# Performance work log

Measured on AMD Instinct MI355X. Metric: run time of the kernel, lower is better.

## Reference

```python
import jax, jax.numpy as jnp
import numpy as np

N_NODES = 714
LRELU = 0.01   # nn.LeakyReLU default
GAT_SLOPE = 0.2  # PyG GATConv internal leaky_relu slope


def _gcn_conv(x, row, col, W, b, n):
    # PyG GCNConv: h = x W; sym-normalized aggregation over edges (self loops already appended)
    h = x @ W
    ones = jnp.ones(row.shape[0], h.dtype)
    deg = jax.ops.segment_sum(ones, col, num_segments=n)
    dinv = jnp.where(deg > 0, jax.lax.rsqrt(deg), 0.0)
    norm = dinv[row] * dinv[col]
    out = jax.ops.segment_sum(h[row] * norm[:, None], col, num_segments=n)
    return out + b


def _gat_conv(x, row, col, W, a_src, a_dst, b, n):
    # PyG GATConv, heads=1: h = x W (no lin bias); edge score = leaky_relu(a_src.h_j + a_dst.h_i)
    h = x @ W
    asrc = h @ a_src
    adst = h @ a_dst
    e = jax.nn.leaky_relu(asrc[row] + adst[col], GAT_SLOPE)
    emax = jax.ops.segment_max(e, col, num_segments=n)
    ee = jnp.exp(e - emax[col])
    denom = jax.ops.segment_sum(ee, col, num_segments=n)
    alpha = ee / (denom[col] + 1e-16)
    out = jax.ops.segment_sum(h[row] * alpha[:, None], col, num_segments=n)
    return out + b


def _forward(feature, edges, poi_tab, cat_tab, lat_tab, long_tab,
             W_in, b_in, gat_W, gat_asrc, gat_adst, gat_b,
             W_out, b_out, W_fc1, b_fc1, W_fc2, b_fc2):
    B, n, _ = feature.shape
    # embedding lookups, concat -> [B, n, 800]
    x = jnp.concatenate([
        poi_tab[feature[..., 0]],
        cat_tab[feature[..., 1]],
        lat_tab[feature[..., 3]],
        long_tab[feature[..., 4]],
    ], axis=-1)
    # append self loops (both GCNConv and GATConv add them by default)
    sl = jnp.arange(n, dtype=edges.dtype)
    sl2 = jnp.broadcast_to(jnp.stack([sl, sl])[None], (B, 2, n))
    ei = jnp.concatenate([edges, sl2], axis=2)  # [B, 2, E+n]
    lrelu = lambda t: jax.nn.leaky_relu(t, LRELU)

    def per_graph(xg, eg):
        row, col = eg[0], eg[1]
        h = lrelu(_gcn_conv(xg, row, col, W_in, b_in, n))
        for i in range(gat_W.shape[0]):  # 3 AGCNUnits, each reuses ONE GATConv twice
            t = _gat_conv(h, row, col, gat_W[i], gat_asrc[i], gat_adst[i], gat_b[i], n)
            h = lrelu(t) + t
            h = lrelu(_gat_conv(h, row, col, gat_W[i], gat_asrc[i], gat_adst[i], gat_b[i], n))
        h = lrelu(_gcn_conv(h, row, col, W_out, b_out, n))  # [n, 1]
        return h[:, 0]

    g = jax.vmap(per_graph)(x, ei)  # [B, n]
    h = jax.nn.leaky_relu(g @ W_fc1 + b_fc1, LRELU)
    return h @ W_fc2 + b_fc2  # [B, 128]


def setup_inputs() -> dict:
    key = jax.random.key(0)
    ks = jax.random.split(key, 20)
    B, E, n = 64, 16384, N_NODES
    C = 128
    feature = jax.random.randint(ks[0], (B, n, 5), 0, 400, dtype=jnp.int64)
    edges = jax.random.randint(ks[1], (B, 2, E), 0, n, dtype=jnp.int64)
    weight = jax.random.normal(ks[2], (B, E, 2), dtype=jnp.float32)
    s = lambda k, shp, fan: (jax.random.normal(k, shp, jnp.float32) / np.sqrt(fan)).astype(jnp.float32)
    return {
        'feature': feature, 'edges': edges, 'weight': weight,
        'poi_tab': s(ks[3], (5099, 300), 1), 'cat_tab': s(ks[4], (400, 100), 1),
        'lat_tab': s(ks[5], (7128, 200), 1), 'long_tab': s(ks[6], (6394, 200), 1),
        'W_in': s(ks[7], (800, C), 800), 'b_in': jnp.zeros((C,), jnp.float32),
        'gat_W': s(ks[8], (3, C, C), C), 'gat_asrc': s(ks[9], (3, C), C),
        'gat_adst': s(ks[10], (3, C), C), 'gat_b': jnp.zeros((3, C), jnp.float32),
        'W_out': s(ks[11], (C, 1), C), 'b_out': jnp.zeros((1,), jnp.float32),
        'W_fc1': s(ks[12], (n, 128), n), 'b_fc1': jnp.zeros((128,), jnp.float32),
        'W_fc2': s(ks[13], (128, 128), 128), 'b_fc2': jnp.zeros((128,), jnp.float32),
    }


def reference(feature, edges, weight, poi_tab, cat_tab, lat_tab, long_tab,
              W_in, b_in, gat_W, gat_asrc, gat_adst, gat_b,
              W_out, b_out, W_fc1, b_fc1, W_fc2, b_fc2):
    # `weight` (edge_attr) is sliced in the original forward but never used in the math
    return _forward(feature, edges, poi_tab, cat_tab, lat_tab, long_tab,
                    W_in, b_in, gat_W, gat_asrc, gat_adst, gat_b,
                    W_out, b_out, W_fc1, b_fc1, W_fc2, b_fc2)
```

## Files before the change

### kernel.cpp

```cpp
#include <hip/hip_runtime.h>


#define BB 64
#define NN 714
#define EE 16384
#define ET (EE + NN)
#define NBt (BB * NN)
#define CC 128
#define RP (NN + 1)
#define DFAST 64
#define KSP 28
#define PROJ_ROWS 19021

typedef _Float16 f16;
typedef __attribute__((ext_vector_type(8))) _Float16 f16x8;
typedef __attribute__((ext_vector_type(4))) _Float16 f16x4;
typedef __attribute__((ext_vector_type(4))) float f32x4;

__device__ __forceinline__ float lrelu01(float x) { return x > 0.f ? x : 0.01f * x; }
__device__ __forceinline__ float lrelu2(float x)  { return x > 0.f ? x : 0.2f  * x; }

__device__ __forceinline__ float wsum(float x) {
#pragma unroll
    for (int o = 32; o > 0; o >>= 1) x += __shfl_xor(x, o);
    return x;
}
__device__ __forceinline__ float wmax(float x) {
#pragma unroll
    for (int o = 32; o > 0; o >>= 1) x = fmaxf(x, __shfl_xor(x, o));
    return x;
}
__device__ __forceinline__ float hsum(float x) {
#pragma unroll
    for (int o = 16; o > 0; o >>= 1) x += __shfl_xor(x, o);
    return x;
}
__device__ __forceinline__ float hmax(float x) {
#pragma unroll
    for (int o = 16; o > 0; o >>= 1) x = fmaxf(x, __shfl_xor(x, o));
    return x;
}

__device__ __forceinline__ int xcd_swz(int bid, int nwg) {
    int q = nwg >> 3, r = nwg & 7;
    int x = bid & 7, l = bid >> 3;
    int base = (x < r) ? x * (q + 1) : r * (q + 1) + (x - r) * q;
    return base + l;
}

__global__ __launch_bounds__(1024) void k_build(
    const int* __restrict__ edges, int* __restrict__ rowptr,
    int* __restrict__ csr_row, float* __restrict__ dinv) {
    __shared__ int degs[NN];
    __shared__ int scan[1024];
    __shared__ int curs[NN];
    int b = blockIdx.x, t = threadIdx.x;
    if (t < NN) degs[t] = 0;
    __syncthreads();
    int rr[17], cc[17];
#pragma unroll
    for (int q = 0; q < 17; ++q) {
        int e = q * 1024 + t;
        int r = -1, c = -1;
        if (e < ET) {
            if (e < EE) { r = edges[b * 2 * EE + e]; c = edges[b * 2 * EE + EE + e]; }
            else        { r = c = e - EE; }
            atomicAdd(&degs[c], 1);
        }
        rr[q] = r; cc[q] = c;
    }
    __syncthreads();
    int cnt = (t < NN) ? degs[t] : 0;
    scan[t] = cnt;
    __syncthreads();
    for (int off = 1; off < 1024; off <<= 1) {
        int val = (t >= off) ? scan[t - off] : 0;
        __syncthreads();
        scan[t] += val;
        __syncthreads();
    }
    if (t < NN) {
        rowptr[b * RP + t + 1] = scan[t];
        curs[t] = scan[t] - cnt;
        dinv[b * NN + t] = cnt > 0 ? rsqrtf((float)cnt) : 0.f;
    }
    if (t == 0) rowptr[b * RP] = 0;
    __syncthreads();
#pragma unroll
    for (int q = 0; q < 17; ++q) {
        if (cc[q] >= 0) {
            int slot = atomicAdd(&curs[cc[q]], 1);
            csr_row[b * ET + slot] = rr[q];
        }
    }
}

#define NSEG (KSP * 8 * 64)
#define NGAT (3 * 4 * 8 * 64)
__global__ void k_prep(const float* __restrict__ W, const float* __restrict__ gat_W,
                       const float* __restrict__ a_s, const float* __restrict__ a_d,
                       f16* __restrict__ BWh, f16* __restrict__ BWl,
                       f16* __restrict__ BGh, f16* __restrict__ BGl,
                       float* __restrict__ wsv, float* __restrict__ wdv) {
    int idx = blockIdx.x * 256 + threadIdx.x;
    if (idx < NSEG) {
        int lane = idx & 63, tc = idx >> 6;
        int ct = tc & 7, ks = tc >> 3;
        int t  = ks < 10 ? 0 : ks < 14 ? 1 : ks < 21 ? 2 : 3;
        int k0 = t == 0 ? 0 : t == 1 ? 10 : t == 2 ? 14 : 21;
        const int Ktab[4] = {300, 100, 200, 200};
        const int Koff[4] = {0, 300, 400, 600};
        int ksl = ks - k0;
        f16x8 ph, pl;
#pragma unroll
        for (int j = 0; j < 8; ++j) {
            int k = ksl * 32 + (lane >> 4) * 8 + j;
            int c = ct * 16 + (lane & 15);
            float v = (k < Ktab[t]) ? W[(size_t)(Koff[t] + k) * CC + c] : 0.f;
            f16 hi = (f16)v;
            ph[j] = hi; pl[j] = (f16)(v - (float)hi);
        }
        *(f16x8*)(BWh + (size_t)idx * 8) = ph;
        *(f16x8*)(BWl + (size_t)idx * 8) = pl;
    } else if (idx < NSEG + NGAT) {
        int i2 = idx - NSEG;
        int lane = i2 & 63, tc = i2 >> 6;
        int ct = tc & 7; tc >>= 3;
        int ks = tc & 3, li = tc >> 2;
        const float* Wl = gat_W + (size_t)li * CC * CC;
        f16x8 ph, pl;
#pragma unroll
        for (int j = 0; j < 8; ++j) {
            int k = ks * 32 + (lane >> 4) * 8 + j;
            int c = ct * 16 + (lane & 15);
            float v = Wl[k * CC + c];
            f16 hi = (f16)v;
            ph[j] = hi; pl[j] = (f16)(v - (float)hi);
        }
        *(f16x8*)(BGh + (size_t)i2 * 8) = ph;
        *(f16x8*)(BGl + (size_t)i2 * 8) = pl;
    } else if (idx < NSEG + NGAT + 3 * CC) {
        int i2 = idx - NSEG - NGAT;
        int i = i2 >> 7, k = i2 & 127;
        const float* Wl = gat_W + (size_t)i * CC * CC;
        float s = 0.f, d = 0.f;
#pragma unroll 4
        for (int c = 0; c < CC; ++c) {
            float w = Wl[k * CC + c];
            s = fmaf(w, a_s[i * CC + c], s);
            d = fmaf(w, a_d[i * CC + c], d);
        }
        wsv[i * CC + k] = s; wdv[i * CC + k] = d;
    }
}

__global__ __launch_bounds__(256) void k_proj(
    const float* __restrict__ poi, const float* __restrict__ cat,
    const float* __restrict__ lat, const float* __restrict__ lon,
    const f16* __restrict__ Bh, const f16* __restrict__ Bl,
    float* __restrict__ P) {
    int bid = blockIdx.x;
    int t, r0;
    if (bid < 160)      { t = 0; r0 = bid * 32; }
    else if (bid < 173) { t = 1; r0 = (bid - 160) * 32; }
    else if (bid < 396) { t = 2; r0 = (bid - 173) * 32; }
    else                { t = 3; r0 = (bid - 396) * 32; }
    const int Ktab[4] = {300, 100, 200, 200};
    const int Rtab[4] = {5099, 400, 7128, 6394};
    const int Rofs[4] = {0, 5099, 5499, 12627};
    const int Kst[4]  = {10, 4, 7, 7};
    const int Bks0[4] = {0, 10, 14, 21};
    const float* tab = t == 0 ? poi : t == 1 ? cat : t == 2 ? lat : lon;
    int K = Ktab[t], R = Rtab[t], nks = Kst[t], bks = Bks0[t];
    int lane = threadIdx.x & 63, w = threadIdx.x >> 6;
    int ct0 = w * 2;
    f32x4 acc[2][2];
#pragma unroll
    for (int rt = 0; rt < 2; ++rt)
#pragma unroll
        for (int c = 0; c < 2; ++c) acc[rt][c] = (f32x4){0.f, 0.f, 0.f, 0.f};

    for (int ks = 0; ks < nks; ++ks) {
        int kbase = ks * 32 + (lane >> 4) * 8;
        f16x8 ah[2], al[2];
#pragma unroll
        for (int rt = 0; rt < 2; ++rt) {
            int row = r0 + rt * 16 + (lane & 15);
            int rowc = row < R ? row : R - 1;
            const float* rp = tab + (size_t)rowc * K;
            float v[8];
            if (kbase + 8 <= K) {
                float4 x0 = ((const float4*)(rp + kbase))[0];
                float4 x1 = ((const float4*)(rp + kbase))[1];
                v[0] = x0.x; v[1] = x0.y; v[2] = x0.z; v[3] = x0.w;
                v[4] = x1.x; v[5] = x1.y; v[6] = x1.z; v[7] = x1.w;
            } else if (kbase >= K) {
#pragma unroll
                for (int m = 0; m < 8; ++m) v[m] = 0.f;
            } else {
#pragma unroll
                for (int m = 0; m < 8; ++m) v[m] = (kbase + m < K) ? rp[kbase + m] : 0.f;
            }
#pragma unroll
            for (int j = 0; j < 8; ++j) {
                f16 hi = (f16)v[j];
                ah[rt][j] = hi; al[rt][j] = (f16)(v[j] - (float)hi);
            }
        }
#pragma unroll
        for (int cti = 0; cti < 2; ++cti) {
            int ct = ct0 + cti;
            f16x8 bh = *(const f16x8*)(Bh + ((size_t)((bks + ks) * 8 + ct) * 64 + lane) * 8);
            f16x8 bl = *(const f16x8*)(Bl + ((size_t)((bks + ks) * 8 + ct) * 64 + lane) * 8);
#pragma unroll
            for (int rt = 0; rt < 2; ++rt) {
                acc[rt][cti] = __builtin_amdgcn_mfma_f32_16x16x32_f16(ah[rt], bh, acc[rt][cti], 0, 0, 0);
                acc[rt][cti] = __builtin_amdgcn_mfma_f32_16x16x32_f16(al[rt], bh, acc[rt][cti], 0, 0, 0);
                acc[rt][cti] = __builtin_amdgcn_mfma_f32_16x16x32_f16(ah[rt], bl, acc[rt][cti], 0, 0, 0);
            }
        }
    }
#pragma unroll
    for (int rt = 0; rt < 2; ++rt)
#pragma unroll
        for (int cti = 0; cti < 2; ++cti)
#pragma unroll
            for (int i = 0; i < 4; ++i) {
                int row = r0 + rt * 16 + (lane >> 4) * 4 + i;
                if (row < R) {
                    int col = (ct0 + cti) * 16 + (lane & 15);
                    P[(size_t)(Rofs[t] + row) * CC + col] = acc[rt][cti][i];
                }
            }
}

__global__ __launch_bounds__(256) void k_assemble(
    const int* __restrict__ feature, const float* __restrict__ P,
    f16* __restrict__ out) {
    int tid = xcd_swz(blockIdx.x, gridDim.x) * 256 + threadIdx.x;
    int g = tid >> 4, c8 = (tid & 15) * 8;
    const int* f = feature + (size_t)g * 5;
    const float4* p0 = (const float4*)(P + (size_t)f[0] * CC + c8);
    const float4* p1 = (const float4*)(P + (size_t)(5099 + f[1]) * CC + c8);
    const float4* p2 = (const float4*)(P + (size_t)(5499 + f[3]) * CC + c8);
    const float4* p3 = (const float4*)(P + (size_t)(12627 + f[4]) * CC + c8);
    float4 a0 = p0[0], a1 = p0[1];
    float4 b0 = p1[0], b1 = p1[1];
    float4 c0 = p2[0], c1 = p2[1];
    float4 d0 = p3[0], d1 = p3[1];
    f16x8 r;
    r[0] = (f16)(a0.x + b0.x + c0.x + d0.x);
    r[1] = (f16)(a0.y + b0.y + c0.y + d0.y);
    r[2] = (f16)(a0.z + b0.z + c0.z + d0.z);
    r[3] = (f16)(a0.w + b0.w + c0.w + d0.w);
    r[4] = (f16)(a1.x + b1.x + c1.x + d1.x);
    r[5] = (f16)(a1.y + b1.y + c1.y + d1.y);
    r[6] = (f16)(a1.z + b1.z + c1.z + d1.z);
    r[7] = (f16)(a1.w + b1.w + c1.w + d1.w);
    *(f16x8*)(out + (size_t)g * CC + c8) = r;
}

__global__ __launch_bounds__(256) void k_gat_gemm(
    const f16* __restrict__ hin, const f16* __restrict__ Bh, const f16* __restrict__ Bl,
    const float* __restrict__ wsv, const float* __restrict__ wdv,
    f16* __restrict__ Hp, float* __restrict__ asrc, float* __restrict__ adst) {
    __shared__ __align__(16) f16 Ah[32 * 128];
    __shared__ float reds[256], redd[256];
    int t = threadIdx.x;
    int g0 = xcd_swz(blockIdx.x, gridDim.x) * 32;
    int lane = t & 63, w = t >> 6;
    int sr = t >> 3, skb = (t & 7) * 16;
    const f16x8* hrow = (const f16x8*)(hin + (size_t)(g0 + sr) * CC + skb);
    f16x8 hv0 = hrow[0], hv1 = hrow[1];
    float ps = 0.f, pd = 0.f;
#pragma unroll
    for (int m = 0; m < 8; ++m) {
        ps = fmaf((float)hv0[m], wsv[skb + m], ps);
        pd = fmaf((float)hv0[m], wdv[skb + m], pd);
        ps = fmaf((float)hv1[m], wsv[skb + 8 + m], ps);
        pd = fmaf((float)hv1[m], wdv[skb + 8 + m], pd);
    }
    {
        int kg0 = (t & 7) * 2;
        int ad0 = sr * 128 + ((kg0 ^ (sr & 7)) << 3);
        int ad1 = sr * 128 + (((kg0 + 1) ^ (sr & 7)) << 3);
        *(f16x8*)&Ah[ad0] = hv0;
        *(f16x8*)&Ah[ad1] = hv1;
    }
    reds[t] = ps; redd[t] = pd;
    __syncthreads();
    if (t < 32) {
        float s = 0.f, d = 0.f;
#pragma unroll
        for (int q = 0; q < 8; ++q) { s += reds[t * 8 + q]; d += redd[t * 8 + q]; }
        asrc[g0 + t] = s; adst[g0 + t] = d;
    }
    f32x4 acc[2][2];
#pragma unroll
    for (int rt = 0; rt < 2; ++rt)
#pragma unroll
        for (int c = 0; c < 2; ++c) acc[rt][c] = (f32x4){0.f, 0.f, 0.f, 0.f};
    int ct0 = w * 2;
#pragma unroll
    for (int ks = 0; ks < 4; ++ks) {
        f16x8 ahf[2];
#pragma unroll
        for (int rt = 0; rt < 2; ++rt) {
            int r = rt * 16 + (lane & 15);
            int kg = (lane >> 4) + ks * 4;
            int ad = r * 128 + ((kg ^ (r & 7)) << 3);
            ahf[rt] = *(const f16x8*)&Ah[ad];
        }
#pragma unroll
        for (int cti = 0; cti < 2; ++cti) {
            int ct = ct0 + cti;
            f16x8 bh = *(const f16x8*)(Bh + ((size_t)(ks * 8 + ct) * 64 + lane) * 8);
            f16x8 bl = *(const f16x8*)(Bl + ((size_t)(ks * 8 + ct) * 64 + lane) * 8);
#pragma unroll
            for (int rt = 0; rt < 2; ++rt) {
                acc[rt][cti] = __builtin_amdgcn_mfma_f32_16x16x32_f16(ahf[rt], bh, acc[rt][cti], 0, 0, 0);
                acc[rt][cti] = __builtin_amdgcn_mfma_f32_16x16x32_f16(ahf[rt], bl, acc[rt][cti], 0, 0, 0);
            }
        }
    }
#pragma unroll
    for (int rt = 0; rt < 2; ++rt)
#pragma unroll
        for (int cti = 0; cti < 2; ++cti)
#pragma unroll
            for (int i = 0; i < 4; ++i) {
                int row = g0 + rt * 16 + (lane >> 4) * 4 + i;
                int col = (ct0 + cti) * 16 + (lane & 15);
                Hp[(size_t)row * CC + col] = (f16)acc[rt][cti][i];
            }
}

template <int MODE>
__global__ __launch_bounds__(256) void k_agg(
    const f16* __restrict__ Hp, const float* __restrict__ aux,
    const float* __restrict__ adst, const int* __restrict__ rowptr,
    const int* __restrict__ csr_row, const float* __restrict__ bias,
    f16* __restrict__ out, const float* __restrict__ Wout, float* __restrict__ pscal) {
    __shared__ float2 pr[4][2][DFAST];
    int wid = threadIdx.x >> 6, lane = threadIdx.x & 63;
    int half = lane >> 5, hl = lane & 31;
    int g = xcd_swz(blockIdx.x, gridDim.x) * 8 + wid * 2 + half;
    int b = g / NN, v = g - b * NN;
    int bN = b * NN, bE = b * ET;
    int s0 = rowptr[b * RP + v], s1 = rowptr[b * RP + v + 1];
    int deg = s1 - s0;

    if (deg <= DFAST) {
        int degp = (deg + 7) & ~7;
        float inv = 1.f;
        int r0 = 0, r1 = 0;
        float w0, w1;
        if (MODE == 2) {
            float dv = aux[g];
            w0 = w1 = 0.f;
            if (hl < deg)      { r0 = csr_row[bE + s0 + hl];      w0 = aux[bN + r0] * dv; }
            if (hl + 32 < deg) { r1 = csr_row[bE + s0 + hl + 32]; w1 = aux[bN + r1] * dv; }
        } else {
            float adv = adst[g];
            float e0 = -3.0e38f, e1 = -3.0e38f;
            if (hl < deg)      { r0 = csr_row[bE + s0 + hl];      e0 = lrelu2(aux[bN + r0] + adv); }
            if (hl + 32 < deg) { r1 = csr_row[bE + s0 + hl + 32]; e1 = lrelu2(aux[bN + r1] + adv); }
            float m = hmax(fmaxf(e0, e1));
            w0 = __expf(e0 - m);
            w1 = __expf(e1 - m);
            float ss = hsum(w0 + w1);
            inv = 1.f / (ss + 1e-16f);
        }
        if (hl < degp)      pr[wid][half][hl]      = make_float2(w0, __int_as_float(r0));
        if (hl + 32 < degp) pr[wid][half][hl + 32] = make_float2(w1, __int_as_float(r1));
        int eh = hl >> 4, ql = hl & 15;
        const f16* Hb = Hp + (size_t)bN * CC;
        float acc0[8], acc1[8], acc2[8], acc3[8];
#pragma unroll
        for (int j = 0; j < 8; ++j) { acc0[j] = 0.f; acc1[j] = 0.f; acc2[j] = 0.f; acc3[j] = 0.f; }
        for (int jj = 0; jj < degp; jj += 8) {
            float2 p0 = pr[wid][half][jj + eh];
            float2 p1 = pr[wid][half][jj + 2 + eh];
            float2 p2 = pr[wid][half][jj + 4 + eh];
            float2 p3 = pr[wid][half][jj + 6 + eh];
            f16x8 h0 = *(const f16x8*)(Hb + (size_t)__float_as_int(p0.y) * CC + ql * 8);
            f16x8 h1 = *(const f16x8*)(Hb + (size_t)__float_as_int(p1.y) * CC + ql * 8);
            f16x8 h2 = *(const f16x8*)(Hb + (size_t)__float_as_int(p2.y) * CC + ql * 8);
            f16x8 h3 = *(const f16x8*)(Hb + (size_t)__float_as_int(p3.y) * CC + ql * 8);
#pragma unroll
            for (int j = 0; j < 8; ++j) {
                acc0[j] = fmaf((float)h0[j], p0.x, acc0[j]);
                acc1[j] = fmaf((float)h1[j], p1.x, acc1[j]);
                acc2[j] = fmaf((float)h2[j], p2.x, acc2[j]);
                acc3[j] = fmaf((float)h3[j], p3.x, acc3[j]);
            }
        }
        float a0[8];
#pragma unroll
        for (int j = 0; j < 8; ++j) {
            float x = acc0[j] + acc1[j] + acc2[j] + acc3[j];
            x += __shfl_xor(x, 16);
            a0[j] = x;
        }
        if (eh == 0) {
            float sc = (MODE == 2) ? 1.f : inv;
            float4 bb0 = ((const float4*)bias)[ql * 2];
            float4 bb1 = ((const float4*)bias)[ql * 2 + 1];
            float tv[8];
            tv[0] = a0[0] * sc + bb0.x; tv[1] = a0[1] * sc + bb0.y;
            tv[2] = a0[2] * sc + bb0.z; tv[3] = a0[3] * sc + bb0.w;
            tv[4] = a0[4] * sc + bb1.x; tv[5] = a0[5] * sc + bb1.y;
            tv[6] = a0[6] * sc + bb1.z; tv[7] = a0[7] * sc + bb1.w;
            float ov[8];
#pragma unroll
            for (int j = 0; j < 8; ++j) {
                float l = lrelu01(tv[j]);
                ov[j] = (MODE == 0) ? l + tv[j] : l;
            }
            if (MODE == 3) {
                float4 w0v = ((const float4*)Wout)[ql * 2];
                float4 w1v = ((const float4*)Wout)[ql * 2 + 1];
                float p = ov[0] * w0v.x + ov[1] * w0v.y + ov[2] * w0v.z + ov[3] * w0v.w
                        + ov[4] * w1v.x + ov[5] * w1v.y + ov[6] * w1v.z + ov[7] * w1v.w;
#pragma unroll
                for (int o = 8; o > 0; o >>= 1) p += __shfl_xor(p, o);
                if (ql == 0) pscal[g] = p;
            } else {
                f16x8 r;
#pragma unroll
                for (int j = 0; j < 8; ++j) r[j] = (f16)ov[j];
                *(f16x8*)(out + (size_t)g * CC + ql * 8) = r;
            }
        }
        return;
    }
    {
        float wsc0 = 0.f;
        float m = 0.f, inv = 1.f, adv = 0.f;
        if (MODE != 2) {
            adv = adst[g];
            m = -3.0e38f;
            for (int j = s0 + hl; j < s1; j += 32)
                m = fmaxf(m, lrelu2(aux[bN + csr_row[bE + j]] + adv));
            m = hmax(m);
            float ssum = 0.f;
            for (int j = s0 + hl; j < s1; j += 32)
                ssum += __expf(lrelu2(aux[bN + csr_row[bE + j]] + adv) - m);
            ssum = hsum(ssum);
            inv = 1.f / (ssum + 1e-16f);
        } else {
            wsc0 = aux[g];
        }
        float x0 = 0.f, x1 = 0.f, x2 = 0.f, x3 = 0.f;
        for (int j = s0; j < s1; ++j) {
            int r = csr_row[bE + j];
            float wj = (MODE == 2) ? aux[bN + r]
                                   : __expf(lrelu2(aux[bN + r] + adv) - m) * inv;
            f16x4 h = *(const f16x4*)(Hp + (size_t)(bN + r) * CC + hl * 4);
            x0 = fmaf(wj, (float)h[0], x0);
            x1 = fmaf(wj, (float)h[1], x1);
            x2 = fmaf(wj, (float)h[2], x2);
            x3 = fmaf(wj, (float)h[3], x3);
        }
        if (MODE == 2) { x0 *= wsc0; x1 *= wsc0; x2 *= wsc0; x3 *= wsc0; }
        float4 bb = ((const float4*)bias)[hl];
        float t0 = x0 + bb.x, t1 = x1 + bb.y, t2 = x2 + bb.z, t3 = x3 + bb.w;
        float l0 = lrelu01(t0), l1 = lrelu01(t1), l2 = lrelu01(t2), l3 = lrelu01(t3);
        float o0 = (MODE == 0) ? l0 + t0 : l0;
        float o1 = (MODE == 0) ? l1 + t1 : l1;
        float o2 = (MODE == 0) ? l2 + t2 : l2;
        float o3 = (MODE == 0) ? l3 + t3 : l3;
        if (MODE == 3) {
            float4 w4 = ((const float4*)Wout)[hl];
            float p = o0 * w4.x + o1 * w4.y + o2 * w4.z + o3 * w4.w;
            p = hsum(p);
            if (hl == 0) pscal[g] = p;
        } else {
            f16x4 r;
            r[0] = (f16)o0; r[1] = (f16)o1; r[2] = (f16)o2; r[3] = (f16)o3;
            *(f16x4*)(out + (size_t)g * CC + hl * 4) = r;
        }
    }
}

__global__ __launch_bounds__(256) void k_out_agg(
    const float* __restrict__ p, const float* __restrict__ dinv,
    const int* __restrict__ rowptr, const int* __restrict__ csr_row,
    const float* __restrict__ bout, float* __restrict__ gv) {
    int wid = threadIdx.x >> 6, lane = threadIdx.x & 63;
    int g = xcd_swz(blockIdx.x, gridDim.x) * 4 + wid;
    int b = g / NN, v = g - b * NN;
    int s0 = rowptr[b * RP + v], s1 = rowptr[b * RP + v + 1];
    float acc = 0.f;
    for (int j = s0 + lane; j < s1; j += 64) {
        int r = csr_row[b * ET + j];
        acc += dinv[b * NN + r] * p[b * NN + r];
    }
    acc = wsum(acc);
    if (lane == 0) gv[g] = lrelu01(acc * dinv[g] + bout[0]);
}

__global__ __launch_bounds__(128) void k_fc(
    const float* __restrict__ gv, const float* __restrict__ W1,
    const float* __restrict__ b1, const float* __restrict__ W2,
    const float* __restrict__ b2, float* __restrict__ outp) {
    __shared__ float gs[NN];
    __shared__ float s1[CC];
    int b = blockIdx.x, tx = threadIdx.x;
    for (int v = tx; v < NN; v += 128) gs[v] = gv[b * NN + v];
    __syncthreads();
    float acc = 0.f;
    for (int v = 0; v < NN; ++v) acc = fmaf(gs[v], W1[v * CC + tx], acc);
    float t = lrelu01(acc + b1[tx]);
    s1[tx] = t;
    __syncthreads();
    float acc2 = 0.f;
#pragma unroll
    for (int k = 0; k < CC; ++k) acc2 = fmaf(s1[k], W2[k * CC + tx], acc2);
    outp[b * CC + tx] = acc2 + b2[tx];
}

extern "C" void kernel_launch(void* const* d_in, const int* in_sizes, int n_in,
                              void* d_out, int out_size, void* d_ws, size_t ws_size,
                              hipStream_t stream) {
    const int*   feature  = (const int*)d_in[0];
    const int*   edges    = (const int*)d_in[1];
    const float* poi      = (const float*)d_in[3];
    const float* cat      = (const float*)d_in[4];
    const float* lat      = (const float*)d_in[5];
    const float* lon      = (const float*)d_in[6];
    const float* W_in     = (const float*)d_in[7];
    const float* b_in     = (const float*)d_in[8];
    const float* gat_W    = (const float*)d_in[9];
    const float* gat_asrc = (const float*)d_in[10];
    const float* gat_adst = (const float*)d_in[11];
    const float* gat_b    = (const float*)d_in[12];
    const float* W_out    = (const float*)d_in[13];
    const float* b_out    = (const float*)d_in[14];
    const float* W_fc1    = (const float*)d_in[15];
    const float* b_fc1    = (const float*)d_in[16];
    const float* W_fc2    = (const float*)d_in[17];
    const float* b_fc2    = (const float*)d_in[18];
    float* outp = (float*)d_out;

    char* ws = (char*)d_ws;
    size_t off = 0;
    auto take = [&](size_t bytes) -> char* {
        char* pp = ws + off;
        off = (off + bytes + 255) & ~(size_t)255;
        return pp;
    };
    int*   csr    = (int*)take((size_t)BB * ET * 4);
    int*   rowptr = (int*)take((size_t)BB * RP * 4);
    float* dinv   = (float*)take((size_t)NBt * 4);
    float* asrc   = (float*)take((size_t)NBt * 4);
    float* adst   = (float*)take((size_t)NBt * 4);
    float* pscal  = (float*)take((size_t)NBt * 4);
    float* gvec   = (float*)take((size_t)NBt * 4);
    f16*   bufA   = (f16*)take((size_t)NBt * CC * 2);
    f16*   bufB   = (f16*)take((size_t)NBt * CC * 2);
    float* P      = (float*)take((size_t)PROJ_ROWS * CC * 4);
    f16*   BWh    = (f16*)take((size_t)KSP * 8 * 64 * 8 * 2);
    f16*   BWl    = (f16*)take((size_t)KSP * 8 * 64 * 8 * 2);
    f16*   BGh    = (f16*)take((size_t)3 * 4 * 8 * 64 * 8 * 2);
    f16*   BGl    = (f16*)take((size_t)3 * 4 * 8 * 64 * 8 * 2);
    float* wsv    = (float*)take((size_t)3 * CC * 4);
    float* wdv    = (float*)take((size_t)3 * CC * 4);

    k_build<<<BB, 1024, 0, stream>>>(edges, rowptr, csr, dinv);

    k_prep<<<(NSEG + NGAT + 3 * CC + 255) / 256, 256, 0, stream>>>(
        W_in, gat_W, gat_asrc, gat_adst, BWh, BWl, BGh, BGl, wsv, wdv);

    k_proj<<<596, 256, 0, stream>>>(poi, cat, lat, lon, BWh, BWl, P);
    k_assemble<<<NBt * 16 / 256, 256, 0, stream>>>(feature, P, bufB);
    k_agg<2><<<NBt / 8, 256, 0, stream>>>(bufB, dinv, nullptr, rowptr, csr, b_in,
                                          bufA, nullptr, nullptr);

    for (int i = 0; i < 3; ++i) {
        const f16* bh = BGh + (size_t)i * 4 * 8 * 64 * 8;
        const f16* bl = BGl + (size_t)i * 4 * 8 * 64 * 8;
        const float* ws_i = wsv + (size_t)i * CC;
        const float* wd_i = wdv + (size_t)i * CC;
        const float* gb = gat_b + (size_t)i * CC;
        k_gat_gemm<<<NBt / 32, 256, 0, stream>>>(bufA, bh, bl, ws_i, wd_i, bufB, asrc, adst);
        k_agg<0><<<NBt / 8, 256, 0, stream>>>(bufB, asrc, adst, rowptr, csr, gb,
                                              bufA, nullptr, nullptr);
        k_gat_gemm<<<NBt / 32, 256, 0, stream>>>(bufA, bh, bl, ws_i, wd_i, bufB, asrc, adst);
        if (i < 2) {
            k_agg<1><<<NBt / 8, 256, 0, stream>>>(bufB, asrc, adst, rowptr, csr, gb,
                                                  bufA, nullptr, nullptr);
        } else {
            k_agg<3><<<NBt / 8, 256, 0, stream>>>(bufB, asrc, adst, rowptr, csr, gb,
                                                  bufA, W_out, pscal);
        }
    }

    k_out_agg<<<NBt / 4, 256, 0, stream>>>(pscal, dinv, rowptr, csr, b_out, gvec);
    k_fc<<<BB, 128, 0, stream>>>(gvec, W_fc1, b_fc1, W_fc2, b_fc2, outp);
}
```

Measured before the change: 299.4 us.

## Fuse graph aggregation with following GAT projection GEMM into one kernel

Each aggregation step now writes its activated output straight into shared memory and immediately runs the next GATConv's weight GEMM and attention-vector dot products. This removes the separate GEMM launches and the round trip of the 128-wide hidden activations through global memory. Attention scores move to ping-pong buffers, and the final GAT aggregation becomes a dedicated kernel. In exchange, each 256-thread block now handles 32 nodes in a serial loop of 4 aggregation iterations before the GEMM, which lowers parallelism and may raise register pressure.

```diff
diff --git a/kernel.cpp b/kernel.cpp
--- a/kernel.cpp
+++ b/kernel.cpp
@@ -23,11 +23,6 @@
 __device__ __forceinline__ float wsum(float x) {
 #pragma unroll
     for (int o = 32; o > 0; o >>= 1) x += __shfl_xor(x, o);
-    return x;
-}
-__device__ __forceinline__ float wmax(float x) {
-#pragma unroll
-    for (int o = 32; o > 0; o >>= 1) x = fmaxf(x, __shfl_xor(x, o));
     return x;
 }
 __device__ __forceinline__ float hsum(float x) {
@@ -260,47 +255,159 @@
     *(f16x8*)(out + (size_t)g * CC + c8) = r;
 }
 
-__global__ __launch_bounds__(256) void k_gat_gemm(
-    const f16* __restrict__ hin, const f16* __restrict__ Bh, const f16* __restrict__ Bl,
+template <int MODE>
+__global__ __launch_bounds__(256) void k_agg_gemm(
+    const f16* __restrict__ Hin, const float* __restrict__ aux,
+    const float* __restrict__ adst, const int* __restrict__ rowptr,
+    const int* __restrict__ csr_row, const float* __restrict__ bias,
+    const f16* __restrict__ Bh, const f16* __restrict__ Bl,
     const float* __restrict__ wsv, const float* __restrict__ wdv,
-    f16* __restrict__ Hp, float* __restrict__ asrc, float* __restrict__ adst) {
+    f16* __restrict__ Hp, float* __restrict__ asrc_o, float* __restrict__ adst_o) {
     __shared__ __align__(16) f16 Ah[32 * 128];
-    __shared__ float reds[256], redd[256];
+    __shared__ float2 pr[4][2][DFAST];
     int t = threadIdx.x;
+    int wid = t >> 6, lane = t & 63;
+    int half = lane >> 5, hl = lane & 31;
     int g0 = xcd_swz(blockIdx.x, gridDim.x) * 32;
-    int lane = t & 63, w = t >> 6;
-    int sr = t >> 3, skb = (t & 7) * 16;
-    const f16x8* hrow = (const f16x8*)(hin + (size_t)(g0 + sr) * CC + skb);
-    f16x8 hv0 = hrow[0], hv1 = hrow[1];
-    float ps = 0.f, pd = 0.f;
-#pragma unroll
-    for (int m = 0; m < 8; ++m) {
-        ps = fmaf((float)hv0[m], wsv[skb + m], ps);
-        pd = fmaf((float)hv0[m], wdv[skb + m], pd);
-        ps = fmaf((float)hv1[m], wsv[skb + 8 + m], ps);
-        pd = fmaf((float)hv1[m], wdv[skb + 8 + m], pd);
-    }
-    {
-        int kg0 = (t & 7) * 2;
-        int ad0 = sr * 128 + ((kg0 ^ (sr & 7)) << 3);
-        int ad1 = sr * 128 + (((kg0 + 1) ^ (sr & 7)) << 3);
-        *(f16x8*)&Ah[ad0] = hv0;
-        *(f16x8*)&Ah[ad1] = hv1;
-    }
-    reds[t] = ps; redd[t] = pd;
+
+    for (int it = 0; it < 4; ++it) {
+        int ln = wid * 2 + half + it * 8;
+        int g = g0 + ln;
+        int b = g / NN, v = g - b * NN;
+        int bN = b * NN, bE = b * ET;
+        int s0 = rowptr[b * RP + v], s1 = rowptr[b * RP + v + 1];
+        int deg = s1 - s0;
+
+        if (deg <= DFAST) {
+            int degp = (deg + 7) & ~7;
+            float inv = 1.f;
+            int r0i = 0, r1i = 0;
+            float w0v, w1v;
+            if (MODE == 2) {
+                float dv = aux[g];
+                w0v = w1v = 0.f;
+                if (hl < deg)      { r0i = csr_row[bE + s0 + hl];      w0v = aux[bN + r0i] * dv; }
+                if (hl + 32 < deg) { r1i = csr_row[bE + s0 + hl + 32]; w1v = aux[bN + r1i] * dv; }
+            } else {
+                float adv = adst[g];
+                float e0 = -3.0e38f, e1 = -3.0e38f;
+                if (hl < deg)      { r0i = csr_row[bE + s0 + hl];      e0 = lrelu2(aux[bN + r0i] + adv); }
+                if (hl + 32 < deg) { r1i = csr_row[bE + s0 + hl + 32]; e1 = lrelu2(aux[bN + r1i] + adv); }
+                float m = hmax(fmaxf(e0, e1));
+                w0v = __expf(e0 - m);
+                w1v = __expf(e1 - m);
+                float ss = hsum(w0v + w1v);
+                inv = 1.f / (ss + 1e-16f);
+            }
+            if (hl < degp)      pr[wid][half][hl]      = make_float2(w0v, __int_as_float(r0i));
+            if (hl + 32 < degp) pr[wid][half][hl + 32] = make_float2(w1v, __int_as_float(r1i));
+            int eh = hl >> 4, ql = hl & 15;
+            const f16* Hb = Hin + (size_t)bN * CC;
+            float acc0[8], acc1[8], acc2[8], acc3[8];
+#pragma unroll
+            for (int j = 0; j < 8; ++j) { acc0[j] = 0.f; acc1[j] = 0.f; acc2[j] = 0.f; acc3[j] = 0.f; }
+            for (int jj = 0; jj < degp; jj += 8) {
+                float2 p0 = pr[wid][half][jj + eh];
+                float2 p1 = pr[wid][half][jj + 2 + eh];
+                float2 p2 = pr[wid][half][jj + 4 + eh];
+                float2 p3 = pr[wid][half][jj + 6 + eh];
+                f16x8 h0 = *(const f16x8*)(Hb + (size_t)__float_as_int(p0.y) * CC + ql * 8);
+                f16x8 h1 = *(const f16x8*)(Hb + (size_t)__float_as_int(p1.y) * CC + ql * 8);
+                f16x8 h2 = *(const f16x8*)(Hb + (size_t)__float_as_int(p2.y) * CC + ql * 8);
+                f16x8 h3 = *(const f16x8*)(Hb + (size_t)__float_as_int(p3.y) * CC + ql * 8);
+#pragma unroll
+                for (int j = 0; j < 8; ++j) {
+                    acc0[j] = fmaf((float)h0[j], p0.x, acc0[j]);
+                    acc1[j] = fmaf((float)h1[j], p1.x, acc1[j]);
+                    acc2[j] = fmaf((float)h2[j], p2.x, acc2[j]);
+                    acc3[j] = fmaf((float)h3[j], p3.x, acc3[j]);
+                }
+            }
+            float ov[8];
+            float sc = (MODE == 2) ? 1.f : inv;
+            float4 bb0 = ((const float4*)bias)[ql * 2];
+            float4 bb1 = ((const float4*)bias)[ql * 2 + 1];
+#pragma unroll
+            for (int j = 0; j < 8; ++j) {
+                float x = acc0[j] + acc1[j] + acc2[j] + acc3[j];
+                x += __shfl_xor(x, 16);
+                float bv = (j < 4) ? ((const float*)&bb0)[j] : ((const float*)&bb1)[j - 4];
+                float tv = x * sc + bv;
+                float l = lrelu01(tv);
+                ov[j] = (MODE == 0) ? l + tv : l;
+            }
+            float ps = 0.f, pd = 0.f;
+#pragma unroll
+            for (int j = 0; j < 8; ++j) {
+                ps = fmaf(ov[j], wsv[ql * 8 + j], ps);
+                pd = fmaf(ov[j], wdv[ql * 8 + j], pd);
+            }
+#pragma unroll
+            for (int o = 8; o > 0; o >>= 1) {
+                ps += __shfl_xor(ps, o);
+                pd += __shfl_xor(pd, o);
+            }
+            if (hl == 0) { asrc_o[g] = ps; adst_o[g] = pd; }
+            if (eh == 0) {
+                f16x8 r;
+#pragma unroll
+                for (int j = 0; j < 8; ++j) r[j] = (f16)ov[j];
+                *(f16x8*)&Ah[ln * 128 + ((ql ^ (ln & 7)) << 3)] = r;
+            }
+        } else {
+            float wsc0 = 0.f, m = 0.f, inv = 1.f, adv = 0.f;
+            if (MODE != 2) {
+                adv = adst[g];
+                m = -3.0e38f;
+                for (int j = s0 + hl; j < s1; j += 32)
+                    m = fmaxf(m, lrelu2(aux[bN + csr_row[bE + j]] + adv));
+                m = hmax(m);
+                float ssum = 0.f;
+                for (int j = s0 + hl; j < s1; j += 32)
+                    ssum += __expf(lrelu2(aux[bN + csr_row[bE + j]] + adv) - m);
+                ssum = hsum(ssum);
+                inv = 1.f / (ssum + 1e-16f);
+            } else {
+                wsc0 = aux[g];
+            }
+            float x0 = 0.f, x1 = 0.f, x2 = 0.f, x3 = 0.f;
+            for (int j = s0; j < s1; ++j) {
+                int r = csr_row[bE + j];
+                float wj = (MODE == 2) ? aux[bN + r]
+                                       : __expf(lrelu2(aux[bN + r] + adv) - m) * inv;
+                f16x4 h = *(const f16x4*)(Hin + (size_t)(bN + r) * CC + hl * 4);
+                x0 = fmaf(wj, (float)h[0], x0);
+                x1 = fmaf(wj, (float)h[1], x1);
+                x2 = fmaf(wj, (float)h[2], x2);
+                x3 = fmaf(wj, (float)h[3], x3);
+            }
+            if (MODE == 2) { x0 *= wsc0; x1 *= wsc0; x2 *= wsc0; x3 *= wsc0; }
+            float4 bb = ((const float4*)bias)[hl];
+            float t0 = x0 + bb.x, t1 = x1 + bb.y, t2 = x2 + bb.z, t3 = x3 + bb.w;
+            float o0 = (MODE == 0) ? lrelu01(t0) + t0 : lrelu01(t0);
+            float o1 = (MODE == 0) ? lrelu01(t1) + t1 : lrelu01(t1);
+            float o2 = (MODE == 0) ? lrelu01(t2) + t2 : lrelu01(t2);
+            float o3 = (MODE == 0) ? lrelu01(t3) + t3 : lrelu01(t3);
+            float4 wsv4 = ((const float4*)wsv)[hl];
+            float4 wdv4 = ((const float4*)wdv)[hl];
+            float ps = o0 * wsv4.x + o1 * wsv4.y + o2 * wsv4.z + o3 * wsv4.w;
+            float pd = o0 * wdv4.x + o1 * wdv4.y + o2 * wdv4.z + o3 * wdv4.w;
+            ps = hsum(ps); pd = hsum(pd);
+            if (hl == 0) { asrc_o[g] = ps; adst_o[g] = pd; }
+            int kg = hl >> 1;
+            f16x4 r;
+            r[0] = (f16)o0; r[1] = (f16)o1; r[2] = (f16)o2; r[3] = (f16)o3;
+            *(f16x4*)&Ah[ln * 128 + ((kg ^ (ln & 7)) << 3) + (hl & 1) * 4] = r;
+        }
+    }
     __syncthreads();
-    if (t < 32) {
-        float s = 0.f, d = 0.f;
-#pragma unroll
-        for (int q = 0; q < 8; ++q) { s += reds[t * 8 + q]; d += redd[t * 8 + q]; }
-        asrc[g0 + t] = s; adst[g0 + t] = d;
-    }
+
     f32x4 acc[2][2];
 #pragma unroll
     for (int rt = 0; rt < 2; ++rt)
 #pragma unroll
         for (int c = 0; c < 2; ++c) acc[rt][c] = (f32x4){0.f, 0.f, 0.f, 0.f};
-    int ct0 = w * 2;
+    int ct0 = wid * 2;
 #pragma unroll
     for (int ks = 0; ks < 4; ++ks) {
         f16x8 ahf[2];
@@ -335,12 +442,11 @@
             }
 }
 
-template <int MODE>
-__global__ __launch_bounds__(256) void k_agg(
-    const f16* __restrict__ Hp, const float* __restrict__ aux,
+__global__ __launch_bounds__(256) void k_agg_last(
+    const f16* __restrict__ Hp, const float* __restrict__ asrc,
     const float* __restrict__ adst, const int* __restrict__ rowptr,
     const int* __restrict__ csr_row, const float* __restrict__ bias,
-    f16* __restrict__ out, const float* __restrict__ Wout, float* __restrict__ pscal) {
+    const float* __restrict__ Wout, float* __restrict__ pscal) {
     __shared__ float2 pr[4][2][DFAST];
     int wid = threadIdx.x >> 6, lane = threadIdx.x & 63;
     int half = lane >> 5, hl = lane & 31;
@@ -352,27 +458,17 @@
 
     if (deg <= DFAST) {
         int degp = (deg + 7) & ~7;
-        float inv = 1.f;
-        int r0 = 0, r1 = 0;
-        float w0, w1;
-        if (MODE == 2) {
-            float dv = aux[g];
-            w0 = w1 = 0.f;
-            if (hl < deg)      { r0 = csr_row[bE + s0 + hl];      w0 = aux[bN + r0] * dv; }
-            if (hl + 32 < deg) { r1 = csr_row[bE + s0 + hl + 32]; w1 = aux[bN + r1] * dv; }
-        } else {
-            float adv = adst[g];
-            float e0 = -3.0e38f, e1 = -3.0e38f;
-            if (hl < deg)      { r0 = csr_row[bE + s0 + hl];      e0 = lrelu2(aux[bN + r0] + adv); }
-            if (hl + 32 < deg) { r1 = csr_row[bE + s0 + hl + 32]; e1 = lrelu2(aux[bN + r1] + adv); }
-            float m = hmax(fmaxf(e0, e1));
-            w0 = __expf(e0 - m);
-            w1 = __expf(e1 - m);
-            float ss = hsum(w0 + w1);
-            inv = 1.f / (ss + 1e-16f);
-        }
-        if (hl < degp)      pr[wid][half][hl]      = make_float2(w0, __int_as_float(r0));
-        if (hl + 32 < degp) pr[wid][half][hl + 32] = make_float2(w1, __int_as_float(r1));
+        float adv = adst[g];
+        float e0 = -3.0e38f, e1 = -3.0e38f;
+        int r0i = 0, r1i = 0;
+        if (hl < deg)      { r0i = csr_row[bE + s0 + hl];      e0 = lrelu2(asrc[bN + r0i] + adv); }
+        if (hl + 32 < deg) { r1i = csr_row[bE + s0 + hl + 32]; e1 = lrelu2(asrc[bN + r1i] + adv); }
+        float m = hmax(fmaxf(e0, e1));
+        float w0v = __expf(e0 - m), w1v = __expf(e1 - m);
+        float ss = hsum(w0v + w1v);
+        float inv = 1.f / (ss + 1e-16f);
+        if (hl < degp)      pr[wid][half][hl]      = make_float2(w0v, __int_as_float(r0i));
+        if (hl + 32 < degp) pr[wid][half][hl + 32] = make_float2(w1v, __int_as_float(r1i));
         int eh = hl >> 4, ql = hl & 15;
         const f16* Hb = Hp + (size_t)bN * CC;
         float acc0[8], acc1[8], acc2[8], acc3[8];
@@ -395,91 +491,53 @@
                 acc3[j] = fmaf((float)h3[j], p3.x, acc3[j]);
             }
         }
-        float a0[8];
+        float4 bb0 = ((const float4*)bias)[ql * 2];
+        float4 bb1 = ((const float4*)bias)[ql * 2 + 1];
+        float4 w0 = ((const float4*)Wout)[ql * 2];
+        float4 w1 = ((const float4*)Wout)[ql * 2 + 1];
+        float p = 0.f;
 #pragma unroll
         for (int j = 0; j < 8; ++j) {
             float x = acc0[j] + acc1[j] + acc2[j] + acc3[j];
             x += __shfl_xor(x, 16);
-            a0[j] = x;
-        }
-        if (eh == 0) {
-            float sc = (MODE == 2) ? 1.f : inv;
-            float4 bb0 = ((const float4*)bias)[ql * 2];
-            float4 bb1 = ((const float4*)bias)[ql * 2 + 1];
-            float tv[8];
-            tv[0] = a0[0] * sc + bb0.x; tv[1] = a0[1] * sc + bb0.y;
-            tv[2] = a0[2] * sc + bb0.z; tv[3] = a0[3] * sc + bb0.w;
-            tv[4] = a0[4] * sc + bb1.x; tv[5] = a0[5] * sc + bb1.y;
-            tv[6] = a0[6] * sc + bb1.z; tv[7] = a0[7] * sc + bb1.w;
-            float ov[8];
-#pragma unroll
-            for (int j = 0; j < 8; ++j) {
-                float l = lrelu01(tv[j]);
-                ov[j] = (MODE == 0) ? l + tv[j] : l;
-            }
-            if (MODE == 3) {
-                float4 w0v = ((const float4*)Wout)[ql * 2];
-                float4 w1v = ((const float4*)Wout)[ql * 2 + 1];
-                float p = ov[0] * w0v.x + ov[1] * w0v.y + ov[2] * w0v.z + ov[3] * w0v.w
-                        + ov[4] * w1v.x + ov[5] * w1v.y + ov[6] * w1v.z + ov[7] * w1v.w;
-#pragma unroll
-                for (int o = 8; o > 0; o >>= 1) p += __shfl_xor(p, o);
-                if (ql == 0) pscal[g] = p;
-            } else {
-                f16x8 r;
-#pragma unroll
-                for (int j = 0; j < 8; ++j) r[j] = (f16)ov[j];
-                *(f16x8*)(out + (size_t)g * CC + ql * 8) = r;
-            }
-        }
+            float bv = (j < 4) ? ((const float*)&bb0)[j] : ((const float*)&bb1)[j - 4];
+            float wv = (j < 4) ? ((const float*)&w0)[j] : ((const float*)&w1)[j - 4];
+            float tv = x * inv + bv;
+            p = fmaf(lrelu01(tv), wv, p);
+        }
+#pragma unroll
+        for (int o = 8; o > 0; o >>= 1) p += __shfl_xor(p, o);
+        if (hl == 0) pscal[g] = p;
         return;
     }
     {
-        float wsc0 = 0.f;
-        float m = 0.f, inv = 1.f, adv = 0.f;
-        if (MODE != 2) {
-            adv = adst[g];
-            m = -3.0e38f;
-            for (int j = s0 + hl; j < s1; j += 32)
-                m = fmaxf(m, lrelu2(aux[bN + csr_row[bE + j]] + adv));
-            m = hmax(m);
-            float ssum = 0.f;
-            for (int j = s0 + hl; j < s1; j += 32)
-                ssum += __expf(lrelu2(aux[bN + csr_row[bE + j]] + adv) - m);
-            ssum = hsum(ssum);
-            inv = 1.f / (ssum + 1e-16f);
-        } else {
-            wsc0 = aux[g];
-        }
+        float adv = adst[g];
+        float m = -3.0e38f;
+        for (int j = s0 + hl; j < s1; j += 32)
+            m = fmaxf(m, lrelu2(asrc[bN + csr_row[bE + j]] + adv));
+        m = hmax(m);
+        float ssum = 0.f;
+        for (int j = s0 + hl; j < s1; j += 32)
+            ssum += __expf(lrelu2(asrc[bN + csr_row[bE + j]] + adv) - m);
+        ssum = hsum(ssum);
+        float inv = 1.f / (ssum + 1e-16f);
         float x0 = 0.f, x1 = 0.f, x2 = 0.f, x3 = 0.f;
         for (int j = s0; j < s1; ++j) {
             int r = csr_row[bE + j];
-            float wj = (MODE == 2) ? aux[bN + r]
-                                   : __expf(lrelu2(aux[bN + r] + adv) - m) * inv;
+            float wj = __expf(lrelu2(asrc[bN + r] + adv) - m) * inv;
             f16x4 h = *(const f16x4*)(Hp + (size_t)(bN + r) * CC + hl * 4);
             x0 = fmaf(wj, (float)h[0], x0);
             x1 = fmaf(wj, (float)h[1], x1);
             x2 = fmaf(wj, (float)h[2], x2);
             x3 = fmaf(wj, (float)h[3], x3);
         }
-        if (MODE == 2) { x0 *= wsc0; x1 *= wsc0; x2 *= wsc0; x3 *= wsc0; }
         float4 bb = ((const float4*)bias)[hl];
         float t0 = x0 + bb.x, t1 = x1 + bb.y, t2 = x2 + bb.z, t3 = x3 + bb.w;
-        float l0 = lrelu01(t0), l1 = lrelu01(t1), l2 = lrelu01(t2), l3 = lrelu01(t3);
-        float o0 = (MODE == 0) ? l0 + t0 : l0;
-        float o1 = (MODE == 0) ? l1 + t1 : l1;
-        float o2 = (MODE == 0) ? l2 + t2 : l2;
-        float o3 = (MODE == 0) ? l3 + t3 : l3;
-        if (MODE == 3) {
-            float4 w4 = ((const float4*)Wout)[hl];
-            float p = o0 * w4.x + o1 * w4.y + o2 * w4.z + o3 * w4.w;
-            p = hsum(p);
-            if (hl == 0) pscal[g] = p;
-        } else {
-            f16x4 r;
-            r[0] = (f16)o0; r[1] = (f16)o1; r[2] = (f16)o2; r[3] = (f16)o3;
-            *(f16x4*)(out + (size_t)g * CC + hl * 4) = r;
-        }
+        float4 w4 = ((const float4*)Wout)[hl];
+        float p = lrelu01(t0) * w4.x + lrelu01(t1) * w4.y
+                + lrelu01(t2) * w4.z + lrelu01(t3) * w4.w;
+        p = hsum(p);
+        if (hl == 0) pscal[g] = p;
     }
 }
 
@@ -555,6 +613,8 @@
     float* dinv   = (float*)take((size_t)NBt * 4);
     float* asrc   = (float*)take((size_t)NBt * 4);
     float* adst   = (float*)take((size_t)NBt * 4);
+    float* asrc2  = (float*)take((size_t)NBt * 4);
+    float* adst2  = (float*)take((size_t)NBt * 4);
     float* pscal  = (float*)take((size_t)NBt * 4);
     float* gvec   = (float*)take((size_t)NBt * 4);
     f16*   bufA   = (f16*)take((size_t)NBt * CC * 2);
@@ -574,8 +634,11 @@
 
     k_proj<<<596, 256, 0, stream>>>(poi, cat, lat, lon, BWh, BWl, P);
     k_assemble<<<NBt * 16 / 256, 256, 0, stream>>>(feature, P, bufB);
-    k_agg<2><<<NBt / 8, 256, 0, stream>>>(bufB, dinv, nullptr, rowptr, csr, b_in,
-                                          bufA, nullptr, nullptr);
+
+    const int GG = NBt / 32;
+    k_agg_gemm<2><<<GG, 256, 0, stream>>>(
+        bufB, dinv, nullptr, rowptr, csr, b_in,
+        BGh, BGl, wsv, wdv, bufA, asrc, adst);
 
     for (int i = 0; i < 3; ++i) {
         const f16* bh = BGh + (size_t)i * 4 * 8 * 64 * 8;
@@ -583,16 +646,20 @@
         const float* ws_i = wsv + (size_t)i * CC;
         const float* wd_i = wdv + (size_t)i * CC;
         const float* gb = gat_b + (size_t)i * CC;
-        k_gat_gemm<<<NBt / 32, 256, 0, stream>>>(bufA, bh, bl, ws_i, wd_i, bufB, asrc, adst);
-        k_agg<0><<<NBt / 8, 256, 0, stream>>>(bufB, asrc, adst, rowptr, csr, gb,
-                                              bufA, nullptr, nullptr);
-        k_gat_gemm<<<NBt / 32, 256, 0, stream>>>(bufA, bh, bl, ws_i, wd_i, bufB, asrc, adst);
+        k_agg_gemm<0><<<GG, 256, 0, stream>>>(
+            bufA, asrc, adst, rowptr, csr, gb,
+            bh, bl, ws_i, wd_i, bufB, asrc2, adst2);
         if (i < 2) {
-            k_agg<1><<<NBt / 8, 256, 0, stream>>>(bufB, asrc, adst, rowptr, csr, gb,
-                                                  bufA, nullptr, nullptr);
+            const f16* bh2 = BGh + (size_t)(i + 1) * 4 * 8 * 64 * 8;
+            const f16* bl2 = BGl + (size_t)(i + 1) * 4 * 8 * 64 * 8;
+            const float* ws2 = wsv + (size_t)(i + 1) * CC;
+            const float* wd2 = wdv + (size_t)(i + 1) * CC;
+            k_agg_gemm<1><<<GG, 256, 0, stream>>>(
+                bufB, asrc2, adst2, rowptr, csr, gb,
+                bh2, bl2, ws2, wd2, bufA, asrc, adst);
         } else {
-            k_agg<3><<<NBt / 8, 256, 0, stream>>>(bufB, asrc, adst, rowptr, csr, gb,
-                                                  bufA, W_out, pscal);
+            k_agg_last<<<NBt / 8, 256, 0, stream>>>(
+                bufB, asrc2, adst2, rowptr, csr, gb, W_out, pscal);
         }
     }
 
```

After: 320.8 us. 7.2% more time.
